# Kernel optimization log

Measured on AMD Instinct MI355X. Metric: run time of the kernel, lower is better.

The kernel has to match this reference:

```python
import jax, jax.numpy as jnp
import numpy as np

B = 1024
D = 512
M = 65536          # num_memory
C = 4096           # num pseudo-label clusters (= labels.max()+1, fixed for jit)
TEMP = 0.05
EPS = 1e-6


def setup_inputs() -> dict:
    key = jax.random.key(0)
    k1, k2, k3, k4 = jax.random.split(key, 4)
    inputs = jax.random.normal(k1, (B, D), dtype=jnp.float32)
    indexes = jax.random.randint(k2, (B,), 0, M, dtype=jnp.int64)
    feats = jax.random.normal(k3, (M, D), dtype=jnp.float32)
    # memory bank stores L2-normalized features (see _update_feature)
    features = feats / jnp.linalg.norm(feats, axis=1, keepdims=True)
    labels = jax.random.randint(k4, (M,), 0, C, dtype=jnp.int64)
    return {"inputs": inputs, "indexes": indexes, "features": features, "labels": labels}


def reference(inputs, indexes, features, labels):
    # F.normalize(inputs, p=2, dim=1)
    x = inputs / jnp.linalg.norm(inputs, axis=1, keepdims=True)
    # HM.forward: inputs @ features.T, then / temp  -> sim over memory slots [B, M]
    sim = (x @ features.T) / TEMP
    # index_add over labels: per-cluster sum of sim columns  -> [C, B]
    sim_c = jax.ops.segment_sum(sim.T, labels, num_segments=C)
    nums = jax.ops.segment_sum(jnp.ones((M,), dtype=sim.dtype), labels, num_segments=C)  # [C]
    cluster_mask = (nums > 0).astype(sim.dtype)                     # [C]
    # mean within cluster; empty clusters divide by 1
    avg = sim_c / jnp.where(nums > 0, nums, 1.0)[:, None]           # [C, B]
    # masked_softmax over clusters, per sample
    vec = avg.T                                                     # [B, C]
    masked_exps = jnp.exp(vec) * cluster_mask[None, :]
    probs = masked_exps / (jnp.sum(masked_exps, axis=1, keepdims=True) + EPS)
    # F.nll_loss(log(probs + eps), targets) with targets = labels[indexes]
    targets = labels[indexes]                                       # [B]
    logp = jnp.log(probs + EPS)
    loss = -jnp.mean(logp[jnp.arange(B), targets])
    return loss
```

## Files before the change

kernel.cpp:

```cpp
#include <hip/hip_runtime.h>
#include <hip/hip_bf16.h>

#define NB 1024
#define ND 512
#define NM 65536
#define NC 4096
#define CAP 128

static constexpr float TEMP = 0.05f;
static constexpr float EPSF = 1e-6f;

typedef __attribute__((ext_vector_type(8))) short short8v;
typedef __attribute__((ext_vector_type(16))) float f32x16;

static __device__ __forceinline__ short f2bf(float f) {
    __hip_bfloat16 h = __float2bfloat16(f);
    return *reinterpret_cast<short*>(&h);
}

__global__ __launch_bounds__(256) void k_norm_init(const float* __restrict__ in,
                                                   const int* __restrict__ indexes,
                                                   const int* __restrict__ labels,
                                                   short* __restrict__ xnb,
                                                   int* __restrict__ tgt,
                                                   float* __restrict__ denom,
                                                   int* __restrict__ cnt) {
    int wid = threadIdx.x >> 6, l = threadIdx.x & 63;
    int b = blockIdx.x * 4 + wid;
    const float4* row = reinterpret_cast<const float4*>(in + (size_t)b * ND) + l * 2;
    float4 v0 = row[0], v1 = row[1];
    float ss = v0.x * v0.x + v0.y * v0.y + v0.z * v0.z + v0.w * v0.w
             + v1.x * v1.x + v1.y * v1.y + v1.z * v1.z + v1.w * v1.w;
#pragma unroll
    for (int m = 1; m < 64; m <<= 1) ss += __shfl_xor(ss, m);
    float inv = 1.0f / sqrtf(ss);
    short8v o;
    o[0] = f2bf(v0.x * inv); o[1] = f2bf(v0.y * inv);
    o[2] = f2bf(v0.z * inv); o[3] = f2bf(v0.w * inv);
    o[4] = f2bf(v1.x * inv); o[5] = f2bf(v1.y * inv);
    o[6] = f2bf(v1.z * inv); o[7] = f2bf(v1.w * inv);
    *reinterpret_cast<short8v*>(xnb + (size_t)b * ND + l * 8) = o;
    if (threadIdx.x < 16) cnt[blockIdx.x * 16 + threadIdx.x] = 0;
    if (l == 0) {
        tgt[b] = labels[indexes[b]];
        denom[b] = 0.f;
    }
}

__global__ __launch_bounds__(256) void k_scatter(const int* __restrict__ labels,
                                                 int* __restrict__ cnt,
                                                 int* __restrict__ idx) {
    int m = blockIdx.x * 256 + threadIdx.x;
    int c = labels[m];
    int pos = atomicAdd(&cnt[c], 1);
    if (pos < CAP) idx[(size_t)c * CAP + pos] = m;
}

__global__ __launch_bounds__(256) void k_gather(const float* __restrict__ feats,
                                                const int* __restrict__ idx,
                                                const int* __restrict__ cnt,
                                                short* __restrict__ Gb) {
    int wid = threadIdx.x >> 6, l = threadIdx.x & 63;
    int c = blockIdx.x * 4 + wid;
    int n = cnt[c];
    if (n > CAP) n = CAP;
    const int* bucket = idx + (size_t)c * CAP;
    int iv = bucket[l];
    float a0[8] = {0, 0, 0, 0, 0, 0, 0, 0};
    float a1[8] = {0, 0, 0, 0, 0, 0, 0, 0};
    int nn = n < 64 ? n : 64;
    int j = 0;
    for (; j + 1 < nn; j += 2) {
        int m0 = __shfl(iv, j);
        int m1 = __shfl(iv, j + 1);
        const float4* r0 = reinterpret_cast<const float4*>(feats + (size_t)m0 * ND + l * 8);
        const float4* r1 = reinterpret_cast<const float4*>(feats + (size_t)m1 * ND + l * 8);
        float4 v00 = r0[0], v01 = r0[1];
        float4 v10 = r1[0], v11 = r1[1];
        a0[0] += v00.x; a0[1] += v00.y; a0[2] += v00.z; a0[3] += v00.w;
        a0[4] += v01.x; a0[5] += v01.y; a0[6] += v01.z; a0[7] += v01.w;
        a1[0] += v10.x; a1[1] += v10.y; a1[2] += v10.z; a1[3] += v10.w;
        a1[4] += v11.x; a1[5] += v11.y; a1[6] += v11.z; a1[7] += v11.w;
    }
    if (j < nn) {
        int m0 = __shfl(iv, j);
        const float4* r0 = reinterpret_cast<const float4*>(feats + (size_t)m0 * ND + l * 8);
        float4 v00 = r0[0], v01 = r0[1];
        a0[0] += v00.x; a0[1] += v00.y; a0[2] += v00.z; a0[3] += v00.w;
        a0[4] += v01.x; a0[5] += v01.y; a0[6] += v01.z; a0[7] += v01.w;
        ++j;
    }
    for (; j < n; ++j) {
        int m0 = bucket[j];
        const float4* r0 = reinterpret_cast<const float4*>(feats + (size_t)m0 * ND + l * 8);
        float4 v00 = r0[0], v01 = r0[1];
        a0[0] += v00.x; a0[1] += v00.y; a0[2] += v00.z; a0[3] += v00.w;
        a0[4] += v01.x; a0[5] += v01.y; a0[6] += v01.z; a0[7] += v01.w;
    }
    short8v o;
#pragma unroll
    for (int i = 0; i < 8; ++i) o[i] = f2bf(a0[i] + a1[i]);
    *reinterpret_cast<short8v*>(Gb + (size_t)c * ND + l * 8) = o;
}

__global__ __launch_bounds__(256) void k_gemm_mfma(const short* __restrict__ A,
                                                   const short* __restrict__ Bm,
                                                   const int* __restrict__ cnt,
                                                   const int* __restrict__ tgt,
                                                   float* __restrict__ denom,
                                                   float* __restrict__ numer) {
    const int tid = threadIdx.x;
    const int w = tid >> 6;
    const int lane = tid & 63;
    const int ln = lane & 31;
    const int kg = lane >> 5;
    const int row0 = blockIdx.y * 128 + (w >> 1) * 64;
    const int col0 = blockIdx.x * 128 + (w & 1) * 64;

    f32x16 acc00 = {}, acc01 = {}, acc10 = {}, acc11 = {};
    const short* pa0 = A + (size_t)(row0 + ln) * ND + kg * 8;
    const short* pa1 = pa0 + 32 * ND;
    const short* pb0 = Bm + (size_t)(col0 + ln) * ND + kg * 8;
    const short* pb1 = pb0 + 32 * ND;
#pragma unroll 8
    for (int k0 = 0; k0 < ND; k0 += 16) {
        short8v a0 = *reinterpret_cast<const short8v*>(pa0 + k0);
        short8v a1 = *reinterpret_cast<const short8v*>(pa1 + k0);
        short8v b0 = *reinterpret_cast<const short8v*>(pb0 + k0);
        short8v b1 = *reinterpret_cast<const short8v*>(pb1 + k0);
        acc00 = __builtin_amdgcn_mfma_f32_32x32x16_bf16(a0, b0, acc00, 0, 0, 0);
        acc01 = __builtin_amdgcn_mfma_f32_32x32x16_bf16(a0, b1, acc01, 0, 0, 0);
        acc10 = __builtin_amdgcn_mfma_f32_32x32x16_bf16(a1, b0, acc10, 0, 0, 0);
        acc11 = __builtin_amdgcn_mfma_f32_32x32x16_bf16(a1, b1, acc11, 0, 0, 0);
    }
    int colA = col0 + ln;
    int colB = colA + 32;
    int nA = cnt[colA], nB = cnt[colB];
    float invA = 1.0f / (TEMP * (float)(nA > 0 ? nA : 1));
    float invB = 1.0f / (TEMP * (float)(nB > 0 ? nB : 1));
    float mA = (nA > 0) ? 1.f : 0.f;
    float mB = (nB > 0) ? 1.f : 0.f;
    int rbase = row0 + 4 * kg;
#pragma unroll
    for (int r = 0; r < 16; ++r) {
        int row = rbase + (r & 3) + 8 * (r >> 2);
        int rowH = row + 32;
        float v00 = acc00[r] * invA, v01 = acc01[r] * invB;
        float v10 = acc10[r] * invA, v11 = acc11[r] * invB;
        int t0 = tgt[row], t1 = tgt[rowH];
        if (t0 == colA) numer[row] = v00;
        if (t0 == colB) numer[row] = v01;
        if (t1 == colA) numer[rowH] = v10;
        if (t1 == colB) numer[rowH] = v11;
        float s0 = mA * __expf(v00) + mB * __expf(v01);
        float s1 = mA * __expf(v10) + mB * __expf(v11);
#pragma unroll
        for (int m = 1; m < 32; m <<= 1) {
            s0 += __shfl_xor(s0, m);
            s1 += __shfl_xor(s1, m);
        }
        if (ln == 0) {
            atomicAdd(&denom[row], s0);
            atomicAdd(&denom[rowH], s1);
        }
    }
}

__global__ __launch_bounds__(256) void k_final(const float* __restrict__ numer,
                                               const float* __restrict__ denom,
                                               float* __restrict__ out) {
    float s = 0.f;
    for (int i = threadIdx.x; i < NB; i += 256) {
        float p = __expf(numer[i]) / (denom[i] + EPSF);
        s += -logf(p + EPSF);
    }
#pragma unroll
    for (int o = 32; o > 0; o >>= 1) s += __shfl_down(s, o);
    __shared__ float sw[4];
    int lane = threadIdx.x & 63, w = threadIdx.x >> 6;
    if (lane == 0) sw[w] = s;
    __syncthreads();
    if (threadIdx.x == 0) out[0] = (sw[0] + sw[1] + sw[2] + sw[3]) / (float)NB;
}

extern "C" void kernel_launch(void* const* d_in, const int* in_sizes, int n_in,
                              void* d_out, int out_size, void* d_ws, size_t ws_size,
                              hipStream_t stream) {
    const float* inputs   = (const float*)d_in[0];
    const int*   indexes  = (const int*)d_in[1];
    const float* features = (const float*)d_in[2];
    const int*   labels   = (const int*)d_in[3];
    float* out = (float*)d_out;

    short* Gb     = (short*)d_ws;
    short* xnb    = Gb + (size_t)NC * ND;
    float* denom  = (float*)(xnb + (size_t)NB * ND);
    float* numer  = denom + NB;
    int*   tgt    = (int*)(numer + NB);
    int*   cnt    = tgt + NB;
    int*   idx    = cnt + NC;

    k_norm_init<<<NB / 4, 256, 0, stream>>>(inputs, indexes, labels, xnb, tgt, denom, cnt);
    k_scatter<<<NM / 256, 256, 0, stream>>>(labels, cnt, idx);
    k_gather<<<NC / 4, 256, 0, stream>>>(features, idx, cnt, Gb);
    dim3 g(NC / 128, NB / 128);
    k_gemm_mfma<<<g, 256, 0, stream>>>(xnb, Gb, cnt, tgt, denom, numer);
    k_final<<<1, 256, 0, stream>>>(numer, denom, out);
}
```

Measured before the change: 74.18 us.

## Fuse pipeline stages into one persistent kernel with software grid barriers

```diff
diff --git a/kernel.cpp b/kernel.cpp
--- a/kernel.cpp
+++ b/kernel.cpp
@@ -18,169 +18,184 @@
     return *reinterpret_cast<short*>(&h);
 }
 
-__global__ __launch_bounds__(256) void k_norm_init(const float* __restrict__ in,
-                                                   const int* __restrict__ indexes,
-                                                   const int* __restrict__ labels,
-                                                   short* __restrict__ xnb,
-                                                   int* __restrict__ tgt,
-                                                   float* __restrict__ denom,
-                                                   int* __restrict__ cnt) {
-    int wid = threadIdx.x >> 6, l = threadIdx.x & 63;
-    int b = blockIdx.x * 4 + wid;
-    const float4* row = reinterpret_cast<const float4*>(in + (size_t)b * ND) + l * 2;
-    float4 v0 = row[0], v1 = row[1];
-    float ss = v0.x * v0.x + v0.y * v0.y + v0.z * v0.z + v0.w * v0.w
-             + v1.x * v1.x + v1.y * v1.y + v1.z * v1.z + v1.w * v1.w;
-#pragma unroll
-    for (int m = 1; m < 64; m <<= 1) ss += __shfl_xor(ss, m);
-    float inv = 1.0f / sqrtf(ss);
-    short8v o;
-    o[0] = f2bf(v0.x * inv); o[1] = f2bf(v0.y * inv);
-    o[2] = f2bf(v0.z * inv); o[3] = f2bf(v0.w * inv);
-    o[4] = f2bf(v1.x * inv); o[5] = f2bf(v1.y * inv);
-    o[6] = f2bf(v1.z * inv); o[7] = f2bf(v1.w * inv);
-    *reinterpret_cast<short8v*>(xnb + (size_t)b * ND + l * 8) = o;
-    if (threadIdx.x < 16) cnt[blockIdx.x * 16 + threadIdx.x] = 0;
-    if (l == 0) {
-        tgt[b] = labels[indexes[b]];
-        denom[b] = 0.f;
-    }
-}
-
-__global__ __launch_bounds__(256) void k_scatter(const int* __restrict__ labels,
-                                                 int* __restrict__ cnt,
-                                                 int* __restrict__ idx) {
-    int m = blockIdx.x * 256 + threadIdx.x;
-    int c = labels[m];
-    int pos = atomicAdd(&cnt[c], 1);
-    if (pos < CAP) idx[(size_t)c * CAP + pos] = m;
-}
-
-__global__ __launch_bounds__(256) void k_gather(const float* __restrict__ feats,
-                                                const int* __restrict__ idx,
-                                                const int* __restrict__ cnt,
-                                                short* __restrict__ Gb) {
-    int wid = threadIdx.x >> 6, l = threadIdx.x & 63;
-    int c = blockIdx.x * 4 + wid;
-    int n = cnt[c];
-    if (n > CAP) n = CAP;
-    const int* bucket = idx + (size_t)c * CAP;
-    int iv = bucket[l];
-    float a0[8] = {0, 0, 0, 0, 0, 0, 0, 0};
-    float a1[8] = {0, 0, 0, 0, 0, 0, 0, 0};
-    int nn = n < 64 ? n : 64;
-    int j = 0;
-    for (; j + 1 < nn; j += 2) {
-        int m0 = __shfl(iv, j);
-        int m1 = __shfl(iv, j + 1);
-        const float4* r0 = reinterpret_cast<const float4*>(feats + (size_t)m0 * ND + l * 8);
-        const float4* r1 = reinterpret_cast<const float4*>(feats + (size_t)m1 * ND + l * 8);
-        float4 v00 = r0[0], v01 = r0[1];
-        float4 v10 = r1[0], v11 = r1[1];
-        a0[0] += v00.x; a0[1] += v00.y; a0[2] += v00.z; a0[3] += v00.w;
-        a0[4] += v01.x; a0[5] += v01.y; a0[6] += v01.z; a0[7] += v01.w;
-        a1[0] += v10.x; a1[1] += v10.y; a1[2] += v10.z; a1[3] += v10.w;
-        a1[4] += v11.x; a1[5] += v11.y; a1[6] += v11.z; a1[7] += v11.w;
-    }
-    if (j < nn) {
-        int m0 = __shfl(iv, j);
-        const float4* r0 = reinterpret_cast<const float4*>(feats + (size_t)m0 * ND + l * 8);
-        float4 v00 = r0[0], v01 = r0[1];
-        a0[0] += v00.x; a0[1] += v00.y; a0[2] += v00.z; a0[3] += v00.w;
-        a0[4] += v01.x; a0[5] += v01.y; a0[6] += v01.z; a0[7] += v01.w;
-        ++j;
-    }
-    for (; j < n; ++j) {
-        int m0 = bucket[j];
-        const float4* r0 = reinterpret_cast<const float4*>(feats + (size_t)m0 * ND + l * 8);
-        float4 v00 = r0[0], v01 = r0[1];
-        a0[0] += v00.x; a0[1] += v00.y; a0[2] += v00.z; a0[3] += v00.w;
-        a0[4] += v01.x; a0[5] += v01.y; a0[6] += v01.z; a0[7] += v01.w;
-    }
-    short8v o;
-#pragma unroll
-    for (int i = 0; i < 8; ++i) o[i] = f2bf(a0[i] + a1[i]);
-    *reinterpret_cast<short8v*>(Gb + (size_t)c * ND + l * 8) = o;
-}
-
-__global__ __launch_bounds__(256) void k_gemm_mfma(const short* __restrict__ A,
-                                                   const short* __restrict__ Bm,
-                                                   const int* __restrict__ cnt,
-                                                   const int* __restrict__ tgt,
-                                                   float* __restrict__ denom,
-                                                   float* __restrict__ numer) {
-    const int tid = threadIdx.x;
-    const int w = tid >> 6;
-    const int lane = tid & 63;
-    const int ln = lane & 31;
-    const int kg = lane >> 5;
-    const int row0 = blockIdx.y * 128 + (w >> 1) * 64;
-    const int col0 = blockIdx.x * 128 + (w & 1) * 64;
-
-    f32x16 acc00 = {}, acc01 = {}, acc10 = {}, acc11 = {};
-    const short* pa0 = A + (size_t)(row0 + ln) * ND + kg * 8;
-    const short* pa1 = pa0 + 32 * ND;
-    const short* pb0 = Bm + (size_t)(col0 + ln) * ND + kg * 8;
-    const short* pb1 = pb0 + 32 * ND;
+__global__ __launch_bounds__(256) void k_init(const int* __restrict__ indexes,
+                                              const int* __restrict__ labels,
+                                              int* __restrict__ cnt,
+                                              float* __restrict__ denom,
+                                              int* __restrict__ tgt,
+                                              int* __restrict__ bar) {
+    int i = blockIdx.x * 256 + threadIdx.x;
+    if (i < NC) cnt[i] = 0;
+    else if (i < NC + NB) denom[i - NC] = 0.f;
+    else if (i < NC + 2 * NB) { int b = i - NC - NB; tgt[b] = labels[indexes[b]]; }
+    else if (i == NC + 2 * NB) bar[0] = 0;
+}
+
+static __device__ __forceinline__ void gbar(int* bar, int target) {
+    __syncthreads();
+    if (threadIdx.x == 0) {
+        __threadfence();
+        atomicAdd(bar, 1);
+        while (atomicAdd(bar, 0) < target) __builtin_amdgcn_s_sleep(8);
+        __threadfence();
+    }
+    __syncthreads();
+}
+
+__global__ __launch_bounds__(256) void k_mega(const float* __restrict__ in,
+                                              const float* __restrict__ feats,
+                                              const int* __restrict__ labels,
+                                              const int* __restrict__ tgt,
+                                              short* __restrict__ xnb,
+                                              short* __restrict__ Gb,
+                                              int* __restrict__ cnt,
+                                              int* __restrict__ idx,
+                                              float* __restrict__ denom,
+                                              float* __restrict__ numer,
+                                              int* __restrict__ bar,
+                                              float* __restrict__ out) {
+    const int b = blockIdx.x;
+    const int t = threadIdx.x;
+    const int wid = t >> 6, l = t & 63;
+
+    {
+        int row = b * 4 + wid;
+        const float4* rp = reinterpret_cast<const float4*>(in + (size_t)row * ND) + l * 2;
+        float4 v0 = rp[0], v1 = rp[1];
+        float ss = v0.x * v0.x + v0.y * v0.y + v0.z * v0.z + v0.w * v0.w
+                 + v1.x * v1.x + v1.y * v1.y + v1.z * v1.z + v1.w * v1.w;
+#pragma unroll
+        for (int m = 1; m < 64; m <<= 1) ss += __shfl_xor(ss, m);
+        float inv = 1.0f / sqrtf(ss);
+        short8v o;
+        o[0] = f2bf(v0.x * inv); o[1] = f2bf(v0.y * inv);
+        o[2] = f2bf(v0.z * inv); o[3] = f2bf(v0.w * inv);
+        o[4] = f2bf(v1.x * inv); o[5] = f2bf(v1.y * inv);
+        o[6] = f2bf(v1.z * inv); o[7] = f2bf(v1.w * inv);
+        *reinterpret_cast<short8v*>(xnb + (size_t)row * ND + l * 8) = o;
+    }
+    {
+        int m = b * 256 + t;
+        int c = labels[m];
+        int pos = atomicAdd(&cnt[c], 1);
+        if (pos < CAP) idx[(size_t)c * CAP + pos] = m;
+    }
+    gbar(bar, 256);
+
+    for (int ci = 0; ci < 4; ++ci) {
+        int c = b * 16 + wid * 4 + ci;
+        int n = cnt[c];
+        if (n > CAP) n = CAP;
+        const int* bucket = idx + (size_t)c * CAP;
+        int iv = bucket[l];
+        float a0[8] = {0, 0, 0, 0, 0, 0, 0, 0};
+        float a1[8] = {0, 0, 0, 0, 0, 0, 0, 0};
+        int nn = n < 64 ? n : 64;
+        int j = 0;
+        for (; j + 1 < nn; j += 2) {
+            int m0 = __shfl(iv, j);
+            int m1 = __shfl(iv, j + 1);
+            const float4* r0 = reinterpret_cast<const float4*>(feats + (size_t)m0 * ND + l * 8);
+            const float4* r1 = reinterpret_cast<const float4*>(feats + (size_t)m1 * ND + l * 8);
+            float4 v00 = r0[0], v01 = r0[1];
+            float4 v10 = r1[0], v11 = r1[1];
+            a0[0] += v00.x; a0[1] += v00.y; a0[2] += v00.z; a0[3] += v00.w;
+            a0[4] += v01.x; a0[5] += v01.y; a0[6] += v01.z; a0[7] += v01.w;
+            a1[0] += v10.x; a1[1] += v10.y; a1[2] += v10.z; a1[3] += v10.w;
+            a1[4] += v11.x; a1[5] += v11.y; a1[6] += v11.z; a1[7] += v11.w;
+        }
+        if (j < nn) {
+            int m0 = __shfl(iv, j);
+            const float4* r0 = reinterpret_cast<const float4*>(feats + (size_t)m0 * ND + l * 8);
+            float4 v00 = r0[0], v01 = r0[1];
+            a0[0] += v00.x; a0[1] += v00.y; a0[2] += v00.z; a0[3] += v00.w;
+            a0[4] += v01.x; a0[5] += v01.y; a0[6] += v01.z; a0[7] += v01.w;
+            ++j;
+        }
+        for (; j < n; ++j) {
+            int m0 = bucket[j];
+            const float4* r0 = reinterpret_cast<const float4*>(feats + (size_t)m0 * ND + l * 8);
+            float4 v00 = r0[0], v01 = r0[1];
+            a0[0] += v00.x; a0[1] += v00.y; a0[2] += v00.z; a0[3] += v00.w;
+            a0[4] += v01.x; a0[5] += v01.y; a0[6] += v01.z; a0[7] += v01.w;
+        }
+        short8v o;
+#pragma unroll
+        for (int i = 0; i < 8; ++i) o[i] = f2bf(a0[i] + a1[i]);
+        *reinterpret_cast<short8v*>(Gb + (size_t)c * ND + l * 8) = o;
+    }
+    gbar(bar, 512);
+
+    {
+        const int bx = b & 31, by = b >> 5;
+        const int w = wid;
+        const int ln = l & 31;
+        const int kg = l >> 5;
+        const int row0 = by * 128 + (w >> 1) * 64;
+        const int col0 = bx * 128 + (w & 1) * 64;
+
+        f32x16 acc00 = {}, acc01 = {}, acc10 = {}, acc11 = {};
+        const short* pa0 = xnb + (size_t)(row0 + ln) * ND + kg * 8;
+        const short* pa1 = pa0 + 32 * ND;
+        const short* pb0 = Gb + (size_t)(col0 + ln) * ND + kg * 8;
+        const short* pb1 = pb0 + 32 * ND;
 #pragma unroll 8
-    for (int k0 = 0; k0 < ND; k0 += 16) {
-        short8v a0 = *reinterpret_cast<const short8v*>(pa0 + k0);
-        short8v a1 = *reinterpret_cast<const short8v*>(pa1 + k0);
-        short8v b0 = *reinterpret_cast<const short8v*>(pb0 + k0);
-        short8v b1 = *reinterpret_cast<const short8v*>(pb1 + k0);
-        acc00 = __builtin_amdgcn_mfma_f32_32x32x16_bf16(a0, b0, acc00, 0, 0, 0);
-        acc01 = __builtin_amdgcn_mfma_f32_32x32x16_bf16(a0, b1, acc01, 0, 0, 0);
-        acc10 = __builtin_amdgcn_mfma_f32_32x32x16_bf16(a1, b0, acc10, 0, 0, 0);
-        acc11 = __builtin_amdgcn_mfma_f32_32x32x16_bf16(a1, b1, acc11, 0, 0, 0);
-    }
-    int colA = col0 + ln;
-    int colB = colA + 32;
-    int nA = cnt[colA], nB = cnt[colB];
-    float invA = 1.0f / (TEMP * (float)(nA > 0 ? nA : 1));
-    float invB = 1.0f / (TEMP * (float)(nB > 0 ? nB : 1));
-    float mA = (nA > 0) ? 1.f : 0.f;
-    float mB = (nB > 0) ? 1.f : 0.f;
-    int rbase = row0 + 4 * kg;
-#pragma unroll
-    for (int r = 0; r < 16; ++r) {
-        int row = rbase + (r & 3) + 8 * (r >> 2);
-        int rowH = row + 32;
-        float v00 = acc00[r] * invA, v01 = acc01[r] * invB;
-        float v10 = acc10[r] * invA, v11 = acc11[r] * invB;
-        int t0 = tgt[row], t1 = tgt[rowH];
-        if (t0 == colA) numer[row] = v00;
-        if (t0 == colB) numer[row] = v01;
-        if (t1 == colA) numer[rowH] = v10;
-        if (t1 == colB) numer[rowH] = v11;
-        float s0 = mA * __expf(v00) + mB * __expf(v01);
-        float s1 = mA * __expf(v10) + mB * __expf(v11);
-#pragma unroll
-        for (int m = 1; m < 32; m <<= 1) {
-            s0 += __shfl_xor(s0, m);
-            s1 += __shfl_xor(s1, m);
-        }
-        if (ln == 0) {
-            atomicAdd(&denom[row], s0);
-            atomicAdd(&denom[rowH], s1);
-        }
-    }
-}
-
-__global__ __launch_bounds__(256) void k_final(const float* __restrict__ numer,
-                                               const float* __restrict__ denom,
-                                               float* __restrict__ out) {
+        for (int k0 = 0; k0 < ND; k0 += 16) {
+            short8v a0 = *reinterpret_cast<const short8v*>(pa0 + k0);
+            short8v a1 = *reinterpret_cast<const short8v*>(pa1 + k0);
+            short8v b0 = *reinterpret_cast<const short8v*>(pb0 + k0);
+            short8v b1 = *reinterpret_cast<const short8v*>(pb1 + k0);
+            acc00 = __builtin_amdgcn_mfma_f32_32x32x16_bf16(a0, b0, acc00, 0, 0, 0);
+            acc01 = __builtin_amdgcn_mfma_f32_32x32x16_bf16(a0, b1, acc01, 0, 0, 0);
+            acc10 = __builtin_amdgcn_mfma_f32_32x32x16_bf16(a1, b0, acc10, 0, 0, 0);
+            acc11 = __builtin_amdgcn_mfma_f32_32x32x16_bf16(a1, b1, acc11, 0, 0, 0);
+        }
+        int colA = col0 + ln;
+        int colB = colA + 32;
+        int nA = cnt[colA], nB = cnt[colB];
+        float invA = 1.0f / (TEMP * (float)(nA > 0 ? nA : 1));
+        float invB = 1.0f / (TEMP * (float)(nB > 0 ? nB : 1));
+        float mA = (nA > 0) ? 1.f : 0.f;
+        float mB = (nB > 0) ? 1.f : 0.f;
+        int rbase = row0 + 4 * kg;
+#pragma unroll
+        for (int r = 0; r < 16; ++r) {
+            int row = rbase + (r & 3) + 8 * (r >> 2);
+            int rowH = row + 32;
+            float v00 = acc00[r] * invA, v01 = acc01[r] * invB;
+            float v10 = acc10[r] * invA, v11 = acc11[r] * invB;
+            int t0 = tgt[row], t1 = tgt[rowH];
+            if (t0 == colA) numer[row] = v00;
+            if (t0 == colB) numer[row] = v01;
+            if (t1 == colA) numer[rowH] = v10;
+            if (t1 == colB) numer[rowH] = v11;
+            float s0 = mA * __expf(v00) + mB * __expf(v01);
+            float s1 = mA * __expf(v10) + mB * __expf(v11);
+#pragma unroll
+            for (int m = 1; m < 32; m <<= 1) {
+                s0 += __shfl_xor(s0, m);
+                s1 += __shfl_xor(s1, m);
+            }
+            if (ln == 0) {
+                atomicAdd(&denom[row], s0);
+                atomicAdd(&denom[rowH], s1);
+            }
+        }
+    }
+    gbar(bar, 768);
+
+    if (b != 0) return;
     float s = 0.f;
-    for (int i = threadIdx.x; i < NB; i += 256) {
+    for (int i = t; i < NB; i += 256) {
         float p = __expf(numer[i]) / (denom[i] + EPSF);
         s += -logf(p + EPSF);
     }
 #pragma unroll
     for (int o = 32; o > 0; o >>= 1) s += __shfl_down(s, o);
     __shared__ float sw[4];
-    int lane = threadIdx.x & 63, w = threadIdx.x >> 6;
-    if (lane == 0) sw[w] = s;
+    if (l == 0) sw[wid] = s;
     __syncthreads();
-    if (threadIdx.x == 0) out[0] = (sw[0] + sw[1] + sw[2] + sw[3]) / (float)NB;
+    if (t == 0) out[0] = (sw[0] + sw[1] + sw[2] + sw[3]) / (float)NB;
 }
 
 extern "C" void kernel_launch(void* const* d_in, const int* in_sizes, int n_in,
@@ -198,12 +213,10 @@
     float* numer  = denom + NB;
     int*   tgt    = (int*)(numer + NB);
     int*   cnt    = tgt + NB;
-    int*   idx    = cnt + NC;
-
-    k_norm_init<<<NB / 4, 256, 0, stream>>>(inputs, indexes, labels, xnb, tgt, denom, cnt);
-    k_scatter<<<NM / 256, 256, 0, stream>>>(labels, cnt, idx);
-    k_gather<<<NC / 4, 256, 0, stream>>>(features, idx, cnt, Gb);
-    dim3 g(NC / 128, NB / 128);
-    k_gemm_mfma<<<g, 256, 0, stream>>>(xnb, Gb, cnt, tgt, denom, numer);
-    k_final<<<1, 256, 0, stream>>>(numer, denom, out);
-}
+    int*   bar    = cnt + NC;
+    int*   idx    = bar + 64;
+
+    k_init<<<25, 256, 0, stream>>>(indexes, labels, cnt, denom, tgt, bar);
+    k_mega<<<256, 256, 0, stream>>>(inputs, features, labels, tgt,
+                                    xnb, Gb, cnt, idx, denom, numer, bar, out);
+}
```

Result: slower. 132.3 us (+78.3%).
